# Kernel optimization log

Measured on AMD Instinct MI355X. Metric: run time of the kernel, lower is better.

Reference implementation:

```python
import jax, jax.numpy as jnp
import numpy as np
from jax import lax

SPATIAL_K = 30
FEATURE_K = 6
EPS = 1e-12  # F.normalize eps


def setup_inputs() -> dict:
    key = jax.random.key(0)
    k1, k2 = jax.random.split(key)
    N, D = 10000, 256
    ema_feat = jax.random.normal(k1, (N, D), dtype=jnp.float32)
    pos = jax.random.randint(k2, (N, 2), 0, 512, dtype=jnp.int64)
    return {"ema_feat": ema_feat, "pos": pos}


def _spatial_candidates(pos, k_spatial):
    # Brute-force k-NN on 2D integer positions (replaces sklearn KD-tree).
    posf = pos.astype(jnp.float32)  # [N, 2]
    sq = jnp.sum(posf * posf, axis=-1)  # [N]
    d2 = sq[:, None] + sq[None, :] - 2.0 * (posf @ posf.T)  # [N, N]
    N = pos.shape[0]
    # exclude self (sklearn returns self first, code drops column 0)
    d2 = d2 + jnp.where(jnp.eye(N, dtype=bool), jnp.inf, 0.0).astype(d2.dtype)
    _, idx = lax.top_k(-d2, k_spatial)  # nearest = largest negative distance
    return idx  # [N, k_spatial]


def reference(ema_feat, pos):
    N = ema_feat.shape[0]
    k_spatial = min(SPATIAL_K, N - 1)
    k_feat = min(FEATURE_K, k_spatial)

    spatial_candidates = _spatial_candidates(pos, k_spatial)  # [N, Ks]

    # F.normalize(ema_feat, dim=-1): x / max(||x||, eps)
    norm = jnp.linalg.norm(ema_feat, axis=-1, keepdims=True)
    feat_norm = ema_feat / jnp.maximum(norm, EPS)  # [N, D]

    cand_feat = feat_norm[spatial_candidates]  # [N, Ks, D]
    sim = jnp.einsum("nd,nkd->nk", feat_norm, cand_feat)  # cosine sim [N, Ks]

    topk_sim, topk_local_idx = lax.top_k(sim, k_feat)  # [N, Kf]
    topk_indices = jnp.take_along_axis(spatial_candidates, topk_local_idx, axis=1)
    topk_weights = jax.nn.softmax(topk_sim, axis=-1)
    return topk_indices, topk_weights
```

## Files before the change

### kernel.cpp

```cpp
#include <hip/hip_runtime.h>
#include <cstdint>
#include <cstddef>

#define FD    256
#define KS    30
#define KF    6
#define CSH   4
#define GW    32
#define NCELLS (GW*GW)
#define BCAP  40
#define OVCAP 128
#define KREG  8
#define SCAPW 96
#define MAXC  100
#define PIPE  5
#define CPB   (BCAP/4)
#define GBLK  (NCELLS*CPB + OVCAP/4)

#define WFENCE() __threadfence_block()

__global__ __launch_bounds__(1024) void zero_kernel(int* __restrict__ cellCnt,
                                                    int* __restrict__ ovfCnt) {
  cellCnt[threadIdx.x] = 0;
  if (threadIdx.x == 0) *ovfCnt = 0;
}

__global__ __launch_bounds__(256) void prep_bin_kernel(const float* __restrict__ x,
                                                       float* __restrict__ y,
                                                       const int2* __restrict__ pos,
                                                       int* __restrict__ cellCnt,
                                                       int2* __restrict__ bucket,
                                                       int* __restrict__ ovfCnt,
                                                       int2* __restrict__ ovf, int N) {
  const int j = blockIdx.x * 256 + threadIdx.x;
  if (j < N) {
    int2 p = pos[j];
    const int cell = (p.y >> CSH) * GW + (p.x >> CSH);
    const int s = atomicAdd(&cellCnt[cell], 1);
    const int2 e = make_int2(p.x | (p.y << 16), j);
    if (s < BCAP) bucket[cell * BCAP + s] = e;
    else { int o = atomicAdd(ovfCnt, 1); if (o < OVCAP) ovf[o] = e; }
  }
  const int row = blockIdx.x * 4 + (threadIdx.x >> 6);
  if (row >= N) return;
  const int lane = threadIdx.x & 63;
  float4 v = ((const float4*)(x + (size_t)row * FD))[lane];
  float ss = v.x * v.x + v.y * v.y + v.z * v.z + v.w * v.w;
#pragma unroll
  for (int o = 32; o; o >>= 1) ss += __shfl_down(ss, o);
  ss = __shfl(ss, 0);
  const float d = fmaxf(sqrtf(ss), 1e-12f);
  float4 o4;
  o4.x = v.x / d; o4.y = v.y / d; o4.z = v.z / d; o4.w = v.w / d;
  ((float4*)(y + (size_t)row * FD))[lane] = o4;
}

__global__ __launch_bounds__(256, 6) void graph_kernel(const int2* __restrict__ pos,
                                                       const int* __restrict__ cellCnt,
                                                       const int2* __restrict__ bucket,
                                                       const int* __restrict__ ovfCnt,
                                                       const int2* __restrict__ ovf,
                                                       const float* __restrict__ fn,
                                                       float* __restrict__ outI,
                                                       float* __restrict__ outW, int N) {
  __shared__ float qf[4][FD];
  __shared__ unsigned long long surv[4][SCAPW];
  __shared__ int pfx[4][MAXC + 1];
  __shared__ int cbase[4][MAXC];
  __shared__ int hist[4][64];
  __shared__ float sims[4][KS];
  __shared__ int selj[4][KS];
  __shared__ int wsel[4][KF];
  __shared__ int kd2[4];

  const int w = threadIdx.x >> 6, lane = threadIdx.x & 63;
  const int b = blockIdx.x;
  const int ovfN = min(*ovfCnt, OVCAP);

  int i;
  if (b < NCELLS * CPB) {
    const int cell = b / CPB;
    const int slot = (b % CPB) * 4 + w;
    if (slot >= min(cellCnt[cell], BCAP)) return;
    i = bucket[cell * BCAP + slot].y;
  } else {
    const int o = (b - NCELLS * CPB) * 4 + w;
    if (o >= ovfN) return;
    i = ovf[o].y;
  }

  float* qfw = qf[w];
  unsigned long long* survw = surv[w];
  int* pfxw = pfx[w];
  int* basew = cbase[w];
  int* histw = hist[w];
  float* simsw = sims[w];
  int* seljw = selj[w];
  int* wselw = wsel[w];

  const int2 q = pos[i];
  const int qx = q.x, qy = q.y;
  const int cx = qx >> CSH, cy = qy >> CSH;

  ((float4*)qfw)[lane] = ((const float4*)(fn + (size_t)i * FD))[lane];
  WFENCE();

  int R = 2;
  int sn = 0;
  for (;;) {
    const int W = 2 * R + 1;
    const int ns = min(W * W, MAXC);
    int run = 0;
    for (int cb = 0; cb < ns; cb += 64) {
      const int s = cb + lane;
      int cnt = 0, base = 0;
      if (s < ns) {
        int dy = s / W - R, dx = s % W - R;
        int yy = cy + dy, xx = cx + dx;
        if (yy >= 0 && yy < GW && xx >= 0 && xx < GW) {
          int cid = yy * GW + xx;
          cnt = min(cellCnt[cid], BCAP);
          base = cid * BCAP;
        }
      }
      int incl = cnt;
#pragma unroll
      for (int o = 1; o < 64; o <<= 1) { int u = __shfl_up(incl, o); if (lane >= o) incl += u; }
      if (s < ns) { pfxw[s] = run + incl - cnt; basew[s] = base; }
      run += __shfl(incl, 63);
    }
    if (lane == 0) pfxw[ns] = run;
    WFENCE();
    const int M = run;
    const int MM = min(M + ovfN, 64 * KREG);

    unsigned long long kreg[KREG];
#pragma unroll
    for (int s8 = 0; s8 < KREG; ++s8) {
      kreg[s8] = ~0ull;
      const int m = lane + 64 * s8;
      if (m < MM) {
        int2 e;
        if (m < M) {
          int c = 0;
#pragma unroll
          for (int st = 64; st; st >>= 1) { int nc = c + st; if (nc < ns && pfxw[nc] <= m) c = nc; }
          e = bucket[basew[c] + (m - pfxw[c])];
        } else {
          e = ovf[m - M];
        }
        const int j = e.y;
        if (j != i) {
          int x = e.x & 0xffff, y = e.x >> 16;
          int dx = qx - x, dy = qy - y;
          unsigned d2 = (unsigned)(dx * dx + dy * dy);
          kreg[s8] = (((unsigned long long)d2) << 16) | (unsigned)j;
        }
      }
    }

    histw[lane] = 0;
    WFENCE();
#pragma unroll
    for (int s8 = 0; s8 < KREG; ++s8)
      if (kreg[s8] != ~0ull)
        atomicAdd(&histw[min((int)(kreg[s8] >> 22), 63)], 1);
    WFENCE();
    int cum = histw[lane];
#pragma unroll
    for (int o = 1; o < 64; o <<= 1) { int u = __shfl_up(cum, o); if (lane >= o) cum += u; }
    const unsigned long long bal = __ballot(cum >= KS);
    unsigned long long Tk;
    if (bal == 0) Tk = 0x7fffffffull << 16;
    else {
      int bb = __ffsll((unsigned long long)bal) - 1;
      Tk = (bb == 63) ? (0x7fffffffull << 16) : (((unsigned long long)(bb + 1) << 6) << 16);
    }

    int sbase = 0;
#pragma unroll
    for (int s8 = 0; s8 < KREG; ++s8) {
      const bool p = kreg[s8] < Tk;
      const unsigned long long mask = __ballot(p);
      if (p) {
        int idx = sbase + __popcll(mask & ((1ull << lane) - 1));
        if (idx < SCAPW) survw[idx] = kreg[s8];
      }
      sbase += __popcll(mask);
    }
    sn = min(sbase, SCAPW);
    WFENCE();

    for (int p = lane; p < sn; p += 64) {
      const unsigned long long kp = survw[p];
      int r = 0;
      for (int s = 0; s < sn; ++s) r += (survw[s] < kp) ? 1 : 0;
      if (r < KS) seljw[r] = (int)(kp & 0xffffu);
      if (r == KS - 1) kd2[w] = (int)(kp >> 16);
    }
    WFENCE();

    bool done = false;
    if (sn >= KS) {
      const int kthd2 = kd2[w];
      int sg = 1 << 15;
      if (cx - R > 0)      sg = min(sg, qx - ((cx - R) << CSH));
      if (cx + R < GW - 1) sg = min(sg, (((cx + R) << CSH) + 15) - qx);
      if (cy - R > 0)      sg = min(sg, qy - ((cy - R) << CSH));
      if (cy + R < GW - 1) sg = min(sg, (((cy + R) << CSH) + 15) - qy);
      done = kthd2 < (sg + 1) * (sg + 1);
    }
    if (done) break;
    ++R;
  }

  const float4 q4v = ((const float4*)qfw)[lane];
  float4 fbuf[PIPE];
#pragma unroll
  for (int c = 0; c < PIPE; ++c)
    fbuf[c] = ((const float4*)(fn + (size_t)seljw[c] * FD))[lane];
#pragma unroll
  for (int c = 0; c < KS; ++c) {
    const float4 f = fbuf[c % PIPE];
    if (c + PIPE < KS)
      fbuf[c % PIPE] = ((const float4*)(fn + (size_t)seljw[c + PIPE] * FD))[lane];
    float d = f.x * q4v.x + f.y * q4v.y + f.z * q4v.z + f.w * q4v.w;
#pragma unroll
    for (int o = 32; o; o >>= 1) d += __shfl_down(d, o);
    if (lane == 0) simsw[c] = d;
  }
  WFENCE();

  if (lane < KS) {
    const float simv = simsw[lane];
    int r = 0;
    for (int s = 0; s < KS; ++s) {
      const float so = simsw[s];
      if (so > simv || (so == simv && s < lane)) ++r;
    }
    if (r < KF) wselw[r] = lane;
  }
  WFENCE();

  if (lane < KF) {
    const float m = simsw[wselw[0]];
    float sum = 0.f, my = 0.f;
#pragma unroll
    for (int r = 0; r < KF; ++r) {
      float e = expf(simsw[wselw[r]] - m);
      sum += e;
      if (r == lane) my = e;
    }
    outI[(size_t)i * KF + lane] = (float)seljw[wselw[lane]];
    outW[(size_t)i * KF + lane] = my / sum;
  }
}

extern "C" void kernel_launch(void* const* d_in, const int* in_sizes, int n_in,
                              void* d_out, int out_size, void* d_ws, size_t ws_size,
                              hipStream_t stream) {
  const float* feat = (const float*)d_in[0];
  const int2* pos = (const int2*)d_in[1];
  const int N = in_sizes[1] / 2;

  char* ws = (char*)d_ws;
  float* fn = (float*)ws;
  size_t off = (size_t)N * FD * sizeof(float);
  int* cellCnt = (int*)(ws + off);  off += NCELLS * sizeof(int);
  int* ovfCnt  = (int*)(ws + off);  off += 2 * sizeof(int);
  int2* bucket = (int2*)(ws + off); off += (size_t)NCELLS * BCAP * sizeof(int2);
  int2* ovf    = (int2*)(ws + off); off += OVCAP * sizeof(int2);

  float* out = (float*)d_out;

  zero_kernel<<<1, 1024, 0, stream>>>(cellCnt, ovfCnt);
  prep_bin_kernel<<<(N + 3) / 4, 256, 0, stream>>>(feat, fn, pos, cellCnt, bucket,
                                                   ovfCnt, ovf, N);
  graph_kernel<<<GBLK, 256, 0, stream>>>(pos, cellCnt, bucket, ovfCnt, ovf, fn,
                                         out, out + (size_t)N * KF, N);
}
```

Baseline: 117.7 us.

## Launch one wavefront per point with prefix-scan cell lookup instead of padded cell slots

The grid was sized as cells × bucket capacity slots, so most blocks and wavefronts exited immediately because cells hold far fewer than 40 points. Now the grid has one wavefront per query. Each wavefront prefix-scans the 1024 cell counts to find which cell and slot its query index falls into, and indices past the total go to the overflow list. The query feature is also kept in registers instead of being staged through shared memory. This removes many empty blocks and trims LDS use, at the cost of a redundant 1024-entry scan in every wavefront.

```diff
diff --git a/kernel.cpp b/kernel.cpp
--- a/kernel.cpp
+++ b/kernel.cpp
@@ -14,8 +14,6 @@
 #define SCAPW 96
 #define MAXC  100
 #define PIPE  5
-#define CPB   (BCAP/4)
-#define GBLK  (NCELLS*CPB + OVCAP/4)
 
 #define WFENCE() __threadfence_block()
 
@@ -63,7 +61,6 @@
                                                        const float* __restrict__ fn,
                                                        float* __restrict__ outI,
                                                        float* __restrict__ outW, int N) {
-  __shared__ float qf[4][FD];
   __shared__ unsigned long long surv[4][SCAPW];
   __shared__ int pfx[4][MAXC + 1];
   __shared__ int cbase[4][MAXC];
@@ -74,22 +71,51 @@
   __shared__ int kd2[4];
 
   const int w = threadIdx.x >> 6, lane = threadIdx.x & 63;
-  const int b = blockIdx.x;
+  const int qi = blockIdx.x * 4 + w;
+  if (qi >= N) return;
   const int ovfN = min(*ovfCnt, OVCAP);
 
   int i;
-  if (b < NCELLS * CPB) {
-    const int cell = b / CPB;
-    const int slot = (b % CPB) * 4 + w;
-    if (slot >= min(cellCnt[cell], BCAP)) return;
-    i = bucket[cell * BCAP + slot].y;
-  } else {
-    const int o = (b - NCELLS * CPB) * 4 + w;
-    if (o >= ovfN) return;
-    i = ovf[o].y;
-  }
-
-  float* qfw = qf[w];
+  {
+    const int4* cc4 = (const int4*)cellCnt;
+    int cnts[4][4], lexcl[4], cbases[4];
+    int runbase = 0;
+#pragma unroll
+    for (int c = 0; c < 4; ++c) {
+      int4 v = cc4[c * 64 + lane];
+      cnts[c][0] = min(v.x, BCAP); cnts[c][1] = min(v.y, BCAP);
+      cnts[c][2] = min(v.z, BCAP); cnts[c][3] = min(v.w, BCAP);
+      int s = cnts[c][0] + cnts[c][1] + cnts[c][2] + cnts[c][3];
+      int incl = s;
+#pragma unroll
+      for (int o = 1; o < 64; o <<= 1) { int u = __shfl_up(incl, o); if (lane >= o) incl += u; }
+      lexcl[c] = incl - s;
+      cbases[c] = runbase;
+      runbase += __shfl(incl, 63);
+    }
+    const int total = runbase;
+    if (qi < total) {
+      int fcell = -1, fslot = 0;
+#pragma unroll
+      for (int c = 0; c < 4; ++c) {
+        int p = cbases[c] + lexcl[c];
+#pragma unroll
+        for (int k = 0; k < 4; ++k) {
+          int cn = cnts[c][k];
+          if (qi >= p && qi < p + cn) { fcell = (c * 64 + lane) * 4 + k; fslot = qi - p; }
+          p += cn;
+        }
+      }
+      const unsigned long long m = __ballot(fcell >= 0);
+      const int src = __ffsll((unsigned long long)m) - 1;
+      fcell = __shfl(fcell, src);
+      fslot = __shfl(fslot, src);
+      i = bucket[fcell * BCAP + fslot].y;
+    } else {
+      i = ovf[qi - total].y;
+    }
+  }
+
   unsigned long long* survw = surv[w];
   int* pfxw = pfx[w];
   int* basew = cbase[w];
@@ -102,8 +128,7 @@
   const int qx = q.x, qy = q.y;
   const int cx = qx >> CSH, cy = qy >> CSH;
 
-  ((float4*)qfw)[lane] = ((const float4*)(fn + (size_t)i * FD))[lane];
-  WFENCE();
+  const float4 q4v = ((const float4*)(fn + (size_t)i * FD))[lane];
 
   int R = 2;
   int sn = 0;
@@ -214,7 +239,6 @@
     ++R;
   }
 
-  const float4 q4v = ((const float4*)qfw)[lane];
   float4 fbuf[PIPE];
 #pragma unroll
   for (int c = 0; c < PIPE; ++c)
@@ -276,6 +300,6 @@
   zero_kernel<<<1, 1024, 0, stream>>>(cellCnt, ovfCnt);
   prep_bin_kernel<<<(N + 3) / 4, 256, 0, stream>>>(feat, fn, pos, cellCnt, bucket,
                                                    ovfCnt, ovf, N);
-  graph_kernel<<<GBLK, 256, 0, stream>>>(pos, cellCnt, bucket, ovfCnt, ovf, fn,
-                                         out, out + (size_t)N * KF, N);
+  graph_kernel<<<(N + 3) / 4, 256, 0, stream>>>(pos, cellCnt, bucket, ovfCnt, ovf, fn,
+                                                out, out + (size_t)N * KF, N);
 }
```

After: 109.2 us. 7.2% less time.

## Compact binned query order to launch dense graph blocks without empty waves

Applied to the files above, without the earlier changes.

Adds a compaction kernel that prefix-sums the per-cell bucket counts and writes a dense, cell-ordered list of query indices, with overflow entries appended at the end. The graph kernel now launches exactly ceil(N/4) blocks and reads its query from that list. Before, it launched one block per four slots of every cell's capacity, and many of those blocks exited early. This removes idle blocks and wavefronts while keeping spatial locality, at the cost of one extra small kernel launch and a workspace array.

```diff
diff --git a/kernel.cpp b/kernel.cpp
--- a/kernel.cpp
+++ b/kernel.cpp
@@ -14,8 +14,6 @@
 #define SCAPW 96
 #define MAXC  100
 #define PIPE  5
-#define CPB   (BCAP/4)
-#define GBLK  (NCELLS*CPB + OVCAP/4)
 
 #define WFENCE() __threadfence_block()
 
@@ -55,11 +53,49 @@
   ((float4*)(y + (size_t)row * FD))[lane] = o4;
 }
 
+__global__ __launch_bounds__(256) void compact_kernel(const int* __restrict__ cellCnt,
+                                                      const int2* __restrict__ bucket,
+                                                      const int* __restrict__ ovfCnt,
+                                                      const int2* __restrict__ ovf,
+                                                      int* __restrict__ qorder, int N) {
+  const int w = threadIdx.x >> 6, lane = threadIdx.x & 63;
+  const int cell = blockIdx.x * 4 + w;
+  const int4* cc4 = (const int4*)cellCnt;
+  int start = 0, total = 0;
+#pragma unroll
+  for (int c = 0; c < 4; ++c) {
+    int4 v = cc4[c * 64 + lane];
+    int s0 = min(v.x, BCAP), s1 = min(v.y, BCAP), s2 = min(v.z, BCAP), s3 = min(v.w, BCAP);
+    int s = s0 + s1 + s2 + s3;
+    int incl = s;
+#pragma unroll
+    for (int o = 1; o < 64; o <<= 1) { int u = __shfl_up(incl, o); if (lane >= o) incl += u; }
+    const int cid0 = (c * 64 + lane) * 4;
+    if (cell >= cid0 && cell < cid0 + 4) {
+      int p = total + (incl - s);
+      if (cell - cid0 > 0) p += s0;
+      if (cell - cid0 > 1) p += s1;
+      if (cell - cid0 > 2) p += s2;
+      start = p;
+    }
+    total += __shfl(incl, 63);
+  }
+  start = __shfl(start, (cell >> 2) & 63);
+  const int cnt = min(cellCnt[cell], BCAP);
+  for (int s = lane; s < cnt; s += 64)
+    qorder[start + s] = bucket[cell * BCAP + s].y;
+  if (cell == NCELLS - 1) {
+    const int on = min(*ovfCnt, OVCAP);
+    for (int o = lane; o < on; o += 64) qorder[total + o] = ovf[o].y;
+  }
+}
+
 __global__ __launch_bounds__(256, 6) void graph_kernel(const int2* __restrict__ pos,
                                                        const int* __restrict__ cellCnt,
                                                        const int2* __restrict__ bucket,
                                                        const int* __restrict__ ovfCnt,
                                                        const int2* __restrict__ ovf,
+                                                       const int* __restrict__ qorder,
                                                        const float* __restrict__ fn,
                                                        float* __restrict__ outI,
                                                        float* __restrict__ outW, int N) {
@@ -74,20 +110,9 @@
   __shared__ int kd2[4];
 
   const int w = threadIdx.x >> 6, lane = threadIdx.x & 63;
-  const int b = blockIdx.x;
-  const int ovfN = min(*ovfCnt, OVCAP);
-
-  int i;
-  if (b < NCELLS * CPB) {
-    const int cell = b / CPB;
-    const int slot = (b % CPB) * 4 + w;
-    if (slot >= min(cellCnt[cell], BCAP)) return;
-    i = bucket[cell * BCAP + slot].y;
-  } else {
-    const int o = (b - NCELLS * CPB) * 4 + w;
-    if (o >= ovfN) return;
-    i = ovf[o].y;
-  }
+  const int qi = blockIdx.x * 4 + w;
+  if (qi >= N) return;
+  const int i = qorder[qi];
 
   float* qfw = qf[w];
   unsigned long long* survw = surv[w];
@@ -101,6 +126,7 @@
   const int2 q = pos[i];
   const int qx = q.x, qy = q.y;
   const int cx = qx >> CSH, cy = qy >> CSH;
+  const int ovfN = min(*ovfCnt, OVCAP);
 
   ((float4*)qfw)[lane] = ((const float4*)(fn + (size_t)i * FD))[lane];
   WFENCE();
@@ -270,12 +296,14 @@
   int* ovfCnt  = (int*)(ws + off);  off += 2 * sizeof(int);
   int2* bucket = (int2*)(ws + off); off += (size_t)NCELLS * BCAP * sizeof(int2);
   int2* ovf    = (int2*)(ws + off); off += OVCAP * sizeof(int2);
+  int* qorder  = (int*)(ws + off);  off += (size_t)N * sizeof(int);
 
   float* out = (float*)d_out;
 
   zero_kernel<<<1, 1024, 0, stream>>>(cellCnt, ovfCnt);
   prep_bin_kernel<<<(N + 3) / 4, 256, 0, stream>>>(feat, fn, pos, cellCnt, bucket,
                                                    ovfCnt, ovf, N);
-  graph_kernel<<<GBLK, 256, 0, stream>>>(pos, cellCnt, bucket, ovfCnt, ovf, fn,
-                                         out, out + (size_t)N * KF, N);
-}
+  compact_kernel<<<NCELLS / 4, 256, 0, stream>>>(cellCnt, bucket, ovfCnt, ovf, qorder, N);
+  graph_kernel<<<(N + 3) / 4, 256, 0, stream>>>(pos, cellCnt, bucket, ovfCnt, ovf, qorder,
+                                                fn, out, out + (size_t)N * KF, N);
+}
```

Result: faster. 111.7 us (-5.1%).
